# Kernel optimization log

Measured on AMD Instinct MI355X. Metric: run time of the kernel, lower is better.

Reference implementation:

```python
import jax, jax.numpy as jnp
import numpy as np
import math

MARGIN = 0.5
SCALE = 64.0
CURVATURE = 1.0
COS_M = math.cos(MARGIN)
SIN_M = math.sin(MARGIN)
TH = math.cos(math.pi - MARGIN)
MM = math.sin(math.pi - MARGIN) * MARGIN

B, D, C = 2048, 512, 16384


def setup_inputs() -> dict:
    key = jax.random.key(0)
    k1, k2, k3 = jax.random.split(key, 3)
    embeddings = jax.random.normal(k1, (B, D), dtype=jnp.float32) * 0.05  # roughly inside the ball
    labels = jax.random.randint(k2, (B,), 0, C)
    # xavier_uniform for [C, D]
    limit = math.sqrt(6.0 / (C + D))
    weight = jax.random.uniform(k3, (C, D), dtype=jnp.float32, minval=-limit, maxval=limit)
    return {"embeddings": embeddings, "labels": labels, "weight": weight}


def _exp_map_zero(v, c):
    sqrt_c = c ** 0.5
    v_norm = jnp.maximum(jnp.linalg.norm(v, axis=-1, keepdims=True), 1e-7)
    return jnp.tanh(sqrt_c * v_norm) * v / (sqrt_c * v_norm)


def reference(embeddings, labels, weight):
    c = CURVATURE
    # class prototypes mapped onto the Poincare ball, clipped to radius 0.95
    proto = _exp_map_zero(weight, c)                                  # [C, D]
    proto_norm = jnp.linalg.norm(proto, axis=-1, keepdims=True)
    proto = jnp.where(proto_norm > 0.95, proto * 0.95 / proto_norm, proto)

    x = embeddings                                                     # [B, D]
    x_sq = jnp.sum(x * x, axis=-1)                                    # [B]
    y_sq = jnp.sum(proto * proto, axis=-1)                            # [C]
    xy = x @ proto.T                                                  # [B, C]
    diff_sq = jnp.maximum(x_sq[:, None] + y_sq[None, :] - 2.0 * xy, 0.0)

    x_sq_c = jnp.minimum(x_sq, 1.0 - 1e-5)
    y_sq_c = jnp.minimum(y_sq, 1.0 - 1e-5)
    denom = (1.0 - c * x_sq_c)[:, None] * (1.0 - c * y_sq_c)[None, :]
    arg = 1.0 + 2.0 * c * diff_sq / jnp.maximum(denom, 1e-7)
    dists = jnp.arccosh(jnp.maximum(arg, 1.0 + 1e-7)) / (c ** 0.5)    # [B, C]

    sims = jnp.exp(-dists)
    cosine = jnp.clip(2.0 * sims - 1.0, -1.0, 1.0)
    sine = jnp.sqrt(jnp.maximum(1.0 - cosine * cosine, 1e-7))
    phi = cosine * COS_M - sine * SIN_M
    phi = jnp.where(cosine > TH, phi, cosine - MM)

    one_hot = jax.nn.one_hot(labels, cosine.shape[1], dtype=cosine.dtype)
    logits = (one_hot * phi + (1.0 - one_hot) * cosine) * SCALE        # [B, C]

    logp = jax.nn.log_softmax(logits, axis=-1)
    loss = -jnp.mean(jnp.take_along_axis(logp, labels[:, None], axis=1))
    return loss
```

## Files before the change

kernel.cpp:

```cpp
#include <hip/hip_runtime.h>
#include <hip/hip_bf16.h>
#include <math.h>

#define Bn 2048
#define Dn 512
#define Cn 16384

typedef float v4f __attribute__((ext_vector_type(4)));

#define WAIT_VM4()  asm volatile("s_waitcnt vmcnt(4)" ::: "memory")
#define WAIT_VM0()  asm volatile("s_waitcnt vmcnt(0)" ::: "memory")
#define LGKM0_BAR() asm volatile("s_waitcnt lgkmcnt(0)\n\ts_barrier" ::: "memory")

__device__ __forceinline__ void async16(const void* g, void* l) {
  __builtin_amdgcn_global_load_lds(
      (const __attribute__((address_space(1))) char*)g,
      (__attribute__((address_space(3))) char*)l, 16, 0, 0);
}

__global__ __launch_bounds__(256) void prep_kernel(
    const float* __restrict__ w, const float* __restrict__ x,
    char* __restrict__ wq8, char* __restrict__ xq8,
    float* __restrict__ fscale, float* __restrict__ ysqA, float* __restrict__ yrA,
    float* __restrict__ xsA, float* __restrict__ xrA)
{
  int gw = (blockIdx.x * 256 + threadIdx.x) >> 6;
  int lane = threadIdx.x & 63;
  bool isW = gw < Cn;
  const float* src = isW ? (w + (size_t)gw * Dn) : (x + (size_t)(gw - Cn) * Dn);
  const float4* s4 = (const float4*)src;
  float4 a = s4[lane * 2], b = s4[lane * 2 + 1];
  float ss = a.x * a.x + a.y * a.y + a.z * a.z + a.w * a.w
           + b.x * b.x + b.y * b.y + b.z * b.z + b.w * b.w;
  #pragma unroll
  for (int d = 1; d < 64; d <<= 1) ss += __shfl_xor(ss, d);

  int w0 = __builtin_amdgcn_cvt_pk_fp8_f32(a.x * 16.f, a.y * 16.f, 0, false);
  w0     = __builtin_amdgcn_cvt_pk_fp8_f32(a.z * 16.f, a.w * 16.f, w0, true);
  int w1 = __builtin_amdgcn_cvt_pk_fp8_f32(b.x * 16.f, b.y * 16.f, 0, false);
  w1     = __builtin_amdgcn_cvt_pk_fp8_f32(b.z * 16.f, b.w * 16.f, w1, true);
  char* dst = isW ? (wq8 + (size_t)gw * Dn) : (xq8 + (size_t)(gw - Cn) * Dn);
  ((int2*)dst)[lane] = make_int2(w0, w1);

  if (lane == 0) {
    if (isW) {
      float n = fmaxf(sqrtf(ss), 1e-7f);
      float t = tanhf(n);
      float tc = fminf(t, 0.95f);
      fscale[gw] = tc / n;
      float ys = tc * tc;
      ysqA[gw] = ys;
      yrA[gw] = 1.f / (1.f - fminf(ys, 1.f - 1e-5f));
    } else {
      int r = gw - Cn;
      xsA[r] = ss;
      xrA[r] = 1.f / (1.f - fminf(ss, 1.f - 1e-5f));
    }
  }
}

__global__ __launch_bounds__(256, 3) void gemm_kernel(
    const char* __restrict__ xq8, const char* __restrict__ wq8,
    const float* __restrict__ fscale, const float* __restrict__ ysqA,
    const float* __restrict__ yrA, const float* __restrict__ xsA,
    const float* __restrict__ xrA, float* __restrict__ partials)
{
  __shared__ int4 ldsv[3072];
  char* lds = (char*)ldsv;

  const int bid = blockIdx.x;
  const int xcd = bid & 7;
  const int loc = bid >> 3;
  const int mt  = loc & 15;
  const int nt  = (xcd << 4) | (loc >> 4);
  const int mBase = mt * 128;
  const int nBase = nt * 128;
  const int tid = threadIdx.x;
  const int lane = tid & 63;
  const int wave = tid >> 6;
  const int quad = lane >> 4;
  const int l16 = lane & 15;
  const int waveM = wave >> 1;
  const int waveN = wave & 1;

  v4f acc[4][4];
  #pragma unroll
  for (int i = 0; i < 4; ++i)
    #pragma unroll
    for (int j = 0; j < 4; ++j)
      acc[i][j] = (v4f){0.f, 0.f, 0.f, 0.f};

  const int s0 = tid, s1 = tid + 256;
  const int r0 = s0 >> 2, c0 = (s0 & 3) ^ ((r0 >> 1) & 3);
  const int r1 = s1 >> 2, c1 = (s1 & 3) ^ ((r1 >> 1) & 3);
  const char* gA0 = xq8 + (size_t)(mBase + r0) * Dn + c0 * 16;
  const char* gA1 = xq8 + (size_t)(mBase + r1) * Dn + c1 * 16;
  const char* gW0 = wq8 + (size_t)(nBase + r0) * Dn + c0 * 16;
  const char* gW1 = wq8 + (size_t)(nBase + r1) * Dn + c1 * 16;
  const int lo0 = s0 * 16, lo1 = s1 * 16;

  const int kx = (l16 >> 1) & 3;
  int aoff[2], boff[2];
  #pragma unroll
  for (int s = 0; s < 2; ++s) {
    int chunk = (2 * s + (quad >> 1)) ^ kx;
    aoff[s] = (waveM * 64 + l16) * 64 + chunk * 16 + (quad & 1) * 8;
    boff[s] = (waveN * 64 + l16) * 64 + chunk * 16 + (quad & 1) * 8;
  }

  #pragma unroll
  for (int t = 0; t < 2; ++t) {
    char* Ab = lds + t * 16384;
    char* Wb = Ab + 8192;
    async16(gA0 + t * 64, Ab + lo0);
    async16(gA1 + t * 64, Ab + lo1);
    async16(gW0 + t * 64, Wb + lo0);
    async16(gW1 + t * 64, Wb + lo1);
  }

  #pragma unroll
  for (int kt = 0; kt < 8; ++kt) {
    const int cur = kt % 3;
    if (kt < 7) { WAIT_VM4(); } else { WAIT_VM0(); }
    LGKM0_BAR();
    char* Ab = lds + cur * 16384;
    char* Wb = Ab + 8192;
    if (kt + 2 < 8) {
      const int nx = (kt + 2) % 3;
      char* An = lds + nx * 16384;
      char* Wn = An + 8192;
      async16(gA0 + (kt + 2) * 64, An + lo0);
      async16(gA1 + (kt + 2) * 64, An + lo1);
      async16(gW0 + (kt + 2) * 64, Wn + lo0);
      async16(gW1 + (kt + 2) * 64, Wn + lo1);
    }
    long af[4][2], bf[4][2];
    #pragma unroll
    for (int s = 0; s < 2; ++s) {
      #pragma unroll
      for (int i = 0; i < 4; ++i) af[i][s] = *(const long*)(Ab + aoff[s] + i * 1024);
      #pragma unroll
      for (int j = 0; j < 4; ++j) bf[j][s] = *(const long*)(Wb + boff[s] + j * 1024);
    }
    #pragma unroll
    for (int s = 0; s < 2; ++s)
      #pragma unroll
      for (int i = 0; i < 4; ++i)
        #pragma unroll
        for (int j = 0; j < 4; ++j)
          acc[i][j] = __builtin_amdgcn_mfma_f32_16x16x32_fp8_fp8(af[i][s], bf[j][s], acc[i][j], 0, 0, 0);
  }

  float ysqj[4], yrj[4], gj[4];
  #pragma unroll
  for (int j = 0; j < 4; ++j) {
    int col = nBase + waveN * 64 + j * 16 + l16;
    gj[j] = -2.f * fscale[col] * (1.f / 256.f);
    ysqj[j] = ysqA[col];
    yrj[j] = yrA[col];
  }
  #pragma unroll
  for (int i = 0; i < 4; ++i) {
    #pragma unroll
    for (int r = 0; r < 4; ++r) {
      int row = mBase + waveM * 64 + i * 16 + quad * 4 + r;
      float xs = xsA[row];
      float xr2 = 2.f * xrA[row];
      float partial = 0.f;
      if (xs >= 0.99999f) {
        #pragma unroll
        for (int j = 0; j < 4; ++j) {
          float d = fmaxf(fmaf(gj[j], acc[i][j][r], xs + ysqj[j]), 0.f);
          float z = fmaf(d, xr2 * yrj[j], 1.f);
          float u = 64.f * __builtin_amdgcn_rcpf(z);
          partial += fmaf(u, fmaf(0.5f, u, 1.f), 1.f);
        }
      } else {
        #pragma unroll
        for (int j = 0; j < 4; ++j) {
          float d = fmaxf(fmaf(gj[j], acc[i][j][r], xs + ysqj[j]), 0.f);
          float z = fmaf(d, xr2 * yrj[j], 1.f);
          float sq = sqrtf(fmaf(z, z, -1.f));
          float u = 128.f * __builtin_amdgcn_rcpf(z + sq);
          partial += __expf(u);
        }
      }
      partial += __shfl_xor(partial, 1);
      partial += __shfl_xor(partial, 2);
      partial += __shfl_xor(partial, 4);
      partial += __shfl_xor(partial, 8);
      if (l16 == 0) partials[(size_t)row * 256 + nt * 2 + waveN] = partial;
    }
  }
}

__global__ __launch_bounds__(256) void final_kernel(
    const float* __restrict__ x, const float* __restrict__ w,
    const int* __restrict__ labels, const float* __restrict__ fscale,
    const float* __restrict__ ysqA, const float* __restrict__ yrA,
    const float* __restrict__ xsA, const float* __restrict__ xrA,
    const float* __restrict__ partials, float* __restrict__ out)
{
  int row = blockIdx.x * 4 + (threadIdx.x >> 6);
  int lane = threadIdx.x & 63;
  const float* pr = partials + (size_t)row * 256;
  float sum = pr[lane] + pr[lane + 64] + pr[lane + 128] + pr[lane + 192];

  int lab = labels[row];
  const float4* xv = (const float4*)(x + (size_t)row * Dn);
  const float4* wv = (const float4*)(w + (size_t)lab * Dn);
  float4 a0 = xv[lane * 2], a1 = xv[lane * 2 + 1];
  float4 b0 = wv[lane * 2], b1 = wv[lane * 2 + 1];
  float dot = a0.x * b0.x + a0.y * b0.y + a0.z * b0.z + a0.w * b0.w
            + a1.x * b1.x + a1.y * b1.y + a1.z * b1.z + a1.w * b1.w;
  #pragma unroll
  for (int d = 1; d < 64; d <<= 1) {
    sum += __shfl_xor(sum, d);
    dot += __shfl_xor(dot, d);
  }

  __shared__ float red[4];
  if (lane == 0) {
    float xy = fscale[lab] * dot;
    float diff = fmaxf(xsA[row] + ysqA[lab] - 2.f * xy, 0.f);
    float z = fmaf(2.f * diff, xrA[row] * yrA[lab], 1.f);
    float sq = sqrtf(fmaf(z, z, -1.f));
    float sims = 1.f / (z + sq);
    float u_lab = 128.f * sims;
    float cosv = fmaf(2.f, sims, -1.f);
    float sine = sqrtf(fmaxf(fmaf(-cosv, cosv, 1.f), 1e-7f));
    float phi = (cosv > -0.8775825619f)
                    ? (cosv * 0.8775825619f - sine * 0.4794255386f)
                    : (cosv - 0.2397127693f);
    float e_lab = __expf(u_lab);
    float e_phi = __expf(fminf(64.f * phi + 64.f, 80.f));
    red[threadIdx.x >> 6] = logf(sum - e_lab + e_phi) - 64.f * phi - 64.f;
  }
  __syncthreads();
  if (threadIdx.x == 0)
    atomicAdd(out, (red[0] + red[1] + red[2] + red[3]) * (1.f / (float)Bn));
}

extern "C" void kernel_launch(void* const* d_in, const int* in_sizes, int n_in,
                              void* d_out, int out_size, void* d_ws, size_t ws_size,
                              hipStream_t stream) {
  (void)in_sizes; (void)n_in; (void)out_size; (void)ws_size;
  const float* emb = (const float*)d_in[0];
  const int* labels = (const int*)d_in[1];
  const float* weight = (const float*)d_in[2];
  float* out = (float*)d_out;

  char* p = (char*)d_ws;
  char* wq8 = p; p += (size_t)Cn * Dn;
  char* xq8 = p; p += (size_t)Bn * Dn;
  float* fscale = (float*)p; p += (size_t)Cn * 4;
  float* ysqA  = (float*)p; p += (size_t)Cn * 4;
  float* yrA   = (float*)p; p += (size_t)Cn * 4;
  float* xsA   = (float*)p; p += (size_t)Bn * 4;
  float* xrA   = (float*)p; p += (size_t)Bn * 4;
  float* partials = (float*)p; p += (size_t)Bn * 256 * 4;

  hipMemsetAsync(out, 0, sizeof(float), stream);
  prep_kernel<<<(Cn + Bn) / 4, 256, 0, stream>>>(weight, emb, wq8, xq8, fscale, ysqA, yrA, xsA, xrA);
  gemm_kernel<<<(Bn / 128) * (Cn / 128), 256, 0, stream>>>(
      xq8, wq8, fscale, ysqA, yrA, xsA, xrA, partials);
  final_kernel<<<Bn / 4, 256, 0, stream>>>(emb, weight, labels, fscale, ysqA, yrA, xsA, xrA, partials, out);
}
```

Measured before the change: 130.0 us.

## Fuse prep, GEMM and final reduction into one cooperative persistent kernel

Replaces the memset plus three launches with a single cooperative kernel of 512 persistent blocks. Grid syncs separate the quantize/prep phase, four GEMM tiles per block, per-row loss terms, and a deterministic final reduction that replaces the atomic. The GEMM pipeline goes from a triple buffer to a double buffer with an extra barrier before each refill, cutting LDS so two blocks fit per CU. This removes launch gaps and tail effects, but limits the GEMM to fewer resident waves and adds grid-wide barrier cost. The old multi-kernel path stays as a fallback if the cooperative launch fails.

```diff
diff --git a/kernel.cpp b/kernel.cpp
--- a/kernel.cpp
+++ b/kernel.cpp
@@ -1,6 +1,8 @@
 #include <hip/hip_runtime.h>
-#include <hip/hip_bf16.h>
+#include <hip/hip_cooperative_groups.h>
 #include <math.h>
+
+namespace cg = cooperative_groups;
 
 #define Bn 2048
 #define Dn 512
@@ -10,6 +12,7 @@
 
 #define WAIT_VM4()  asm volatile("s_waitcnt vmcnt(4)" ::: "memory")
 #define WAIT_VM0()  asm volatile("s_waitcnt vmcnt(0)" ::: "memory")
+#define RAW_BAR()   asm volatile("s_barrier" ::: "memory")
 #define LGKM0_BAR() asm volatile("s_waitcnt lgkmcnt(0)\n\ts_barrier" ::: "memory")
 
 __device__ __forceinline__ void async16(const void* g, void* l) {
@@ -18,16 +21,15 @@
       (__attribute__((address_space(3))) char*)l, 16, 0, 0);
 }
 
-__global__ __launch_bounds__(256) void prep_kernel(
-    const float* __restrict__ w, const float* __restrict__ x,
+
+__device__ __forceinline__ void prep_row(
+    int row, int lane, const float* __restrict__ w, const float* __restrict__ x,
     char* __restrict__ wq8, char* __restrict__ xq8,
     float* __restrict__ fscale, float* __restrict__ ysqA, float* __restrict__ yrA,
     float* __restrict__ xsA, float* __restrict__ xrA)
 {
-  int gw = (blockIdx.x * 256 + threadIdx.x) >> 6;
-  int lane = threadIdx.x & 63;
-  bool isW = gw < Cn;
-  const float* src = isW ? (w + (size_t)gw * Dn) : (x + (size_t)(gw - Cn) * Dn);
+  bool isW = row < Cn;
+  const float* src = isW ? (w + (size_t)row * Dn) : (x + (size_t)(row - Cn) * Dn);
   const float4* s4 = (const float4*)src;
   float4 a = s4[lane * 2], b = s4[lane * 2 + 1];
   float ss = a.x * a.x + a.y * a.y + a.z * a.z + a.w * a.w
@@ -39,7 +41,7 @@
   w0     = __builtin_amdgcn_cvt_pk_fp8_f32(a.z * 16.f, a.w * 16.f, w0, true);
   int w1 = __builtin_amdgcn_cvt_pk_fp8_f32(b.x * 16.f, b.y * 16.f, 0, false);
   w1     = __builtin_amdgcn_cvt_pk_fp8_f32(b.z * 16.f, b.w * 16.f, w1, true);
-  char* dst = isW ? (wq8 + (size_t)gw * Dn) : (xq8 + (size_t)(gw - Cn) * Dn);
+  char* dst = isW ? (wq8 + (size_t)row * Dn) : (xq8 + (size_t)(row - Cn) * Dn);
   ((int2*)dst)[lane] = make_int2(w0, w1);
 
   if (lane == 0) {
@@ -47,41 +49,37 @@
       float n = fmaxf(sqrtf(ss), 1e-7f);
       float t = tanhf(n);
       float tc = fminf(t, 0.95f);
-      fscale[gw] = tc / n;
+      fscale[row] = tc / n;
       float ys = tc * tc;
-      ysqA[gw] = ys;
-      yrA[gw] = 1.f / (1.f - fminf(ys, 1.f - 1e-5f));
+      ysqA[row] = ys;
+      yrA[row] = 1.f / (1.f - fminf(ys, 1.f - 1e-5f));
     } else {
-      int r = gw - Cn;
+      int r = row - Cn;
       xsA[r] = ss;
       xrA[r] = 1.f / (1.f - fminf(ss, 1.f - 1e-5f));
     }
   }
 }
 
-__global__ __launch_bounds__(256, 3) void gemm_kernel(
+__device__ __forceinline__ void gemm_job(
+    int job, int tid, char* lds,
     const char* __restrict__ xq8, const char* __restrict__ wq8,
     const float* __restrict__ fscale, const float* __restrict__ ysqA,
     const float* __restrict__ yrA, const float* __restrict__ xsA,
     const float* __restrict__ xrA, float* __restrict__ partials)
 {
-  __shared__ int4 ldsv[3072];
-  char* lds = (char*)ldsv;
-
-  const int bid = blockIdx.x;
-  const int xcd = bid & 7;
-  const int loc = bid >> 3;
+  const int xcd = job & 7;
+  const int loc = job >> 3;
   const int mt  = loc & 15;
   const int nt  = (xcd << 4) | (loc >> 4);
   const int mBase = mt * 128;
   const int nBase = nt * 128;
-  const int tid = threadIdx.x;
   const int lane = tid & 63;
-  const int wave = tid >> 6;
+  const int wv = tid >> 6;
   const int quad = lane >> 4;
   const int l16 = lane & 15;
-  const int waveM = wave >> 1;
-  const int waveN = wave & 1;
+  const int waveM = wv >> 1;
+  const int waveN = wv & 1;
 
   v4f acc[4][4];
   #pragma unroll
@@ -120,20 +118,11 @@
 
   #pragma unroll
   for (int kt = 0; kt < 8; ++kt) {
-    const int cur = kt % 3;
+    const int cur = kt & 1;
     if (kt < 7) { WAIT_VM4(); } else { WAIT_VM0(); }
-    LGKM0_BAR();
+    RAW_BAR();
     char* Ab = lds + cur * 16384;
     char* Wb = Ab + 8192;
-    if (kt + 2 < 8) {
-      const int nx = (kt + 2) % 3;
-      char* An = lds + nx * 16384;
-      char* Wn = An + 8192;
-      async16(gA0 + (kt + 2) * 64, An + lo0);
-      async16(gA1 + (kt + 2) * 64, An + lo1);
-      async16(gW0 + (kt + 2) * 64, Wn + lo0);
-      async16(gW1 + (kt + 2) * 64, Wn + lo1);
-    }
     long af[4][2], bf[4][2];
     #pragma unroll
     for (int s = 0; s < 2; ++s) {
@@ -149,6 +138,13 @@
         #pragma unroll
         for (int j = 0; j < 4; ++j)
           acc[i][j] = __builtin_amdgcn_mfma_f32_16x16x32_fp8_fp8(af[i][s], bf[j][s], acc[i][j], 0, 0, 0);
+    LGKM0_BAR();
+    if (kt + 2 < 8) {
+      async16(gA0 + (kt + 2) * 64, Ab + lo0);
+      async16(gA1 + (kt + 2) * 64, Ab + lo1);
+      async16(gW0 + (kt + 2) * 64, Wb + lo0);
+      async16(gW1 + (kt + 2) * 64, Wb + lo1);
+    }
   }
 
   float ysqj[4], yrj[4], gj[4];
@@ -194,23 +190,22 @@
   }
 }
 
-__global__ __launch_bounds__(256) void final_kernel(
+__device__ __forceinline__ float final_row_term(
+    int row, int lane,
     const float* __restrict__ x, const float* __restrict__ w,
     const int* __restrict__ labels, const float* __restrict__ fscale,
     const float* __restrict__ ysqA, const float* __restrict__ yrA,
     const float* __restrict__ xsA, const float* __restrict__ xrA,
-    const float* __restrict__ partials, float* __restrict__ out)
-{
-  int row = blockIdx.x * 4 + (threadIdx.x >> 6);
-  int lane = threadIdx.x & 63;
+    const float* __restrict__ partials)
+{
   const float* pr = partials + (size_t)row * 256;
   float sum = pr[lane] + pr[lane + 64] + pr[lane + 128] + pr[lane + 192];
 
   int lab = labels[row];
   const float4* xv = (const float4*)(x + (size_t)row * Dn);
-  const float4* wv = (const float4*)(w + (size_t)lab * Dn);
+  const float4* wv4 = (const float4*)(w + (size_t)lab * Dn);
   float4 a0 = xv[lane * 2], a1 = xv[lane * 2 + 1];
-  float4 b0 = wv[lane * 2], b1 = wv[lane * 2 + 1];
+  float4 b0 = wv4[lane * 2], b1 = wv4[lane * 2 + 1];
   float dot = a0.x * b0.x + a0.y * b0.y + a0.z * b0.z + a0.w * b0.w
             + a1.x * b1.x + a1.y * b1.y + a1.z * b1.z + a1.w * b1.w;
   #pragma unroll
@@ -219,7 +214,7 @@
     dot += __shfl_xor(dot, d);
   }
 
-  __shared__ float red[4];
+  float term = 0.f;
   if (lane == 0) {
     float xy = fscale[lab] * dot;
     float diff = fmaxf(xsA[row] + ysqA[lab] - 2.f * xy, 0.f);
@@ -234,8 +229,86 @@
                     : (cosv - 0.2397127693f);
     float e_lab = __expf(u_lab);
     float e_phi = __expf(fminf(64.f * phi + 64.f, 80.f));
-    red[threadIdx.x >> 6] = logf(sum - e_lab + e_phi) - 64.f * phi - 64.f;
-  }
+    term = logf(sum - e_lab + e_phi) - 64.f * phi - 64.f;
+  }
+  return term;
+}
+
+__global__ __launch_bounds__(256, 2) void fused_kernel(
+    const float* __restrict__ w, const float* __restrict__ x,
+    const int* __restrict__ labels,
+    char* __restrict__ wq8, char* __restrict__ xq8,
+    float* __restrict__ fscale, float* __restrict__ ysqA, float* __restrict__ yrA,
+    float* __restrict__ xsA, float* __restrict__ xrA,
+    float* __restrict__ partials, float* __restrict__ terms, float* __restrict__ out)
+{
+  __shared__ int4 ldsv[2048];
+  char* lds = (char*)ldsv;
+  cg::grid_group grid = cg::this_grid();
+  const int tid = threadIdx.x, lane = tid & 63, wv = tid >> 6;
+
+  for (int row = (blockIdx.x << 2) | wv; row < Cn + Bn; row += 2048)
+    prep_row(row, lane, w, x, wq8, xq8, fscale, ysqA, yrA, xsA, xrA);
+  grid.sync();
+
+  #pragma unroll 1
+  for (int t = 0; t < 4; ++t)
+    gemm_job(blockIdx.x + t * 512, tid, lds, xq8, wq8, fscale, ysqA, yrA, xsA, xrA, partials);
+  grid.sync();
+
+  {
+    int row = blockIdx.x * 4 + wv;
+    float term = final_row_term(row, lane, x, w, labels, fscale, ysqA, yrA, xsA, xrA, partials);
+    float* red = (float*)lds;
+    if (lane == 0) red[wv] = term;
+    __syncthreads();
+    if (tid == 0) terms[blockIdx.x] = red[0] + red[1] + red[2] + red[3];
+  }
+  grid.sync();
+
+  if (blockIdx.x == 0) {
+    float a = terms[tid] + terms[tid + 256];
+    #pragma unroll
+    for (int d = 1; d < 64; d <<= 1) a += __shfl_xor(a, d);
+    float* red = (float*)lds;
+    if (lane == 0) red[wv] = a;
+    __syncthreads();
+    if (tid == 0) out[0] = (red[0] + red[1] + red[2] + red[3]) * (1.f / (float)Bn);
+  }
+}
+
+__global__ __launch_bounds__(256) void prep_kernel(
+    const float* __restrict__ w, const float* __restrict__ x,
+    char* __restrict__ wq8, char* __restrict__ xq8,
+    float* __restrict__ fscale, float* __restrict__ ysqA, float* __restrict__ yrA,
+    float* __restrict__ xsA, float* __restrict__ xrA)
+{
+  int row = (blockIdx.x * 256 + threadIdx.x) >> 6;
+  prep_row(row, threadIdx.x & 63, w, x, wq8, xq8, fscale, ysqA, yrA, xsA, xrA);
+}
+
+__global__ __launch_bounds__(256, 3) void gemm_kernel(
+    const char* __restrict__ xq8, const char* __restrict__ wq8,
+    const float* __restrict__ fscale, const float* __restrict__ ysqA,
+    const float* __restrict__ yrA, const float* __restrict__ xsA,
+    const float* __restrict__ xrA, float* __restrict__ partials)
+{
+  __shared__ int4 ldsv[2048];
+  gemm_job(blockIdx.x, threadIdx.x, (char*)ldsv, xq8, wq8, fscale, ysqA, yrA, xsA, xrA, partials);
+}
+
+__global__ __launch_bounds__(256) void final_kernel(
+    const float* __restrict__ x, const float* __restrict__ w,
+    const int* __restrict__ labels, const float* __restrict__ fscale,
+    const float* __restrict__ ysqA, const float* __restrict__ yrA,
+    const float* __restrict__ xsA, const float* __restrict__ xrA,
+    const float* __restrict__ partials, float* __restrict__ out)
+{
+  int row = blockIdx.x * 4 + (threadIdx.x >> 6);
+  float term = final_row_term(row, threadIdx.x & 63, x, w, labels, fscale,
+                              ysqA, yrA, xsA, xrA, partials);
+  __shared__ float red[4];
+  if ((threadIdx.x & 63) == 0) red[threadIdx.x >> 6] = term;
   __syncthreads();
   if (threadIdx.x == 0)
     atomicAdd(out, (red[0] + red[1] + red[2] + red[3]) * (1.f / (float)Bn));
@@ -259,10 +332,29 @@
   float* xsA   = (float*)p; p += (size_t)Bn * 4;
   float* xrA   = (float*)p; p += (size_t)Bn * 4;
   float* partials = (float*)p; p += (size_t)Bn * 256 * 4;
-
-  hipMemsetAsync(out, 0, sizeof(float), stream);
-  prep_kernel<<<(Cn + Bn) / 4, 256, 0, stream>>>(weight, emb, wq8, xq8, fscale, ysqA, yrA, xsA, xrA);
-  gemm_kernel<<<(Bn / 128) * (Cn / 128), 256, 0, stream>>>(
-      xq8, wq8, fscale, ysqA, yrA, xsA, xrA, partials);
-  final_kernel<<<Bn / 4, 256, 0, stream>>>(emb, weight, labels, fscale, ysqA, yrA, xsA, xrA, partials, out);
-}
+  float* terms = (float*)p; p += 512 * 4;
+
+  int dev = 0;
+  hipGetDevice(&dev);
+  int coopAttr = 0;
+  hipDeviceGetAttribute(&coopAttr, hipDeviceAttributeCooperativeLaunch, dev);
+  int maxPerCU = 0;
+  hipOccupancyMaxActiveBlocksPerMultiprocessor(&maxPerCU, (const void*)fused_kernel, 256, 0);
+
+  hipError_t le = hipErrorUnknown;
+  if (coopAttr == 1 && maxPerCU >= 2) {
+    void* args[] = {(void*)&weight, (void*)&emb, (void*)&labels,
+                    (void*)&wq8, (void*)&xq8, (void*)&fscale, (void*)&ysqA,
+                    (void*)&yrA, (void*)&xsA, (void*)&xrA,
+                    (void*)&partials, (void*)&terms, (void*)&out};
+    le = hipLaunchCooperativeKernel((const void*)fused_kernel, dim3(512), dim3(256),
+                                    args, 0, stream);
+  }
+  if (le != hipSuccess) {
+    hipMemsetAsync(out, 0, sizeof(float), stream);
+    prep_kernel<<<(Cn + Bn) / 4, 256, 0, stream>>>(weight, emb, wq8, xq8, fscale, ysqA, yrA, xsA, xrA);
+    gemm_kernel<<<(Bn / 128) * (Cn / 128), 256, 0, stream>>>(
+        xq8, wq8, fscale, ysqA, yrA, xsA, xrA, partials);
+    final_kernel<<<Bn / 4, 256, 0, stream>>>(emb, weight, labels, fscale, ysqA, yrA, xsA, xrA, partials, out);
+  }
+}
```

New measurement: 126.6 us. 2.6% less time.
